# Optimization experiments

Hardware: AMD Instinct MI355X
Metric: run time of the kernel (lower is better)

## Reference

```python
import jax, jax.numpy as jnp
import numpy as np

B, T, D, K = 8, 4096, 1024, 3


def setup_inputs() -> dict:
    key = jax.random.key(0)
    k0, k1, k2 = jax.random.split(key, 3)
    x = jax.random.normal(k0, (B, T, D), dtype=jnp.float32)
    lim = 1.0 / np.sqrt(D)
    Wv = jax.random.uniform(k1, (D, D), dtype=jnp.float32, minval=-lim, maxval=lim)
    bv = jnp.zeros((D,), dtype=jnp.float32)
    Wo = jax.random.uniform(k2, (D, D), dtype=jnp.float32, minval=-lim, maxval=lim)
    bo = jnp.zeros((D,), dtype=jnp.float32)
    neighbor_weights = jnp.ones((K,), dtype=jnp.float32) / K
    return {"x": x, "Wv": Wv, "bv": bv, "Wo": Wo, "bo": bo,
            "neighbor_weights": neighbor_weights}


def reference(x, Wv, bv, Wo, bo, neighbor_weights):
    # x: [B, T, D]; faithful translation of the unfold -> Linear -> weighted-sum chain
    k = neighbor_weights.shape[0]
    pad = k // 2
    t = x.shape[1]
    # replicate padding along T (torch F.pad mode='replicate')
    xp = jnp.pad(x, ((0, 0), (pad, pad), (0, 0)), mode='edge')  # [B, T+2*pad, D]
    # sliding windows: [B, T, K, D] (small fixed K loop, not a data-dim loop)
    windows = jnp.stack([xp[:, i:i + t, :] for i in range(k)], axis=2)
    # value projection applied per window element (nn.Linear: x @ W.T + b)
    v = jnp.einsum('btkd,ed->btke', windows, Wv) + bv  # [B, T, K, D]
    # fixed-weight neighbor average
    attended = jnp.einsum('btkd,k->btd', v, neighbor_weights)  # [B, T, D]
    # output projection
    return jnp.einsum('btd,ed->bte', attended, Wo) + bo
```

## Files before the change

### kernel.cpp

```cpp
#include <hip/hip_runtime.h>
#include <stdint.h>
#include <stddef.h>

typedef _Float16 f16_t;
typedef _Float16 f16x4 __attribute__((ext_vector_type(4)));
typedef _Float16 f16x8 __attribute__((ext_vector_type(8)));
typedef float f32x4 __attribute__((ext_vector_type(4)));

#define AS_G __attribute__((address_space(1)))
#define AS_L __attribute__((address_space(3)))

__device__ __forceinline__ void gload_lds16(const void* g, void* l) {
  __builtin_amdgcn_global_load_lds((AS_G void*)g, (AS_L void*)l, 16, 0, 0);
}

#define FENCE() asm volatile("" ::: "memory")
#define BARX()                            \
  do {                                    \
    FENCE();                              \
    __builtin_amdgcn_s_barrier();         \
    FENCE();                              \
  } while (0)
#define VMCNT(n) asm volatile("s_waitcnt vmcnt(" #n ")" ::: "memory")


__global__ __launch_bounds__(256) void prep_w_kernel(
    const float* __restrict__ Wo, const float* __restrict__ Wv,
    const float* __restrict__ bv, const float* __restrict__ bo,
    const float* __restrict__ nw, int Kw,
    f16_t* __restrict__ Wo_h, f16_t* __restrict__ WvT, float* __restrict__ bc) {
  __shared__ float smem[32 * 33];
  const int b = blockIdx.x;
  const int t = threadIdx.x;
  if (b < 1024) {
    const int i = b * 256 + t;
    f32x4 v = ((const f32x4*)Wo)[i];
    f16x4 o;
    o.x = (f16_t)v.x; o.y = (f16_t)v.y; o.z = (f16_t)v.z; o.w = (f16_t)v.w;
    ((f16x4*)Wo_h)[i] = o;
  } else if (b < 2048) {
    const int i = b - 1024;
    const int bx = i & 31, by = i >> 5;
    const int tx = t & 31, ty = t >> 5;
#pragma unroll
    for (int k = 0; k < 32; k += 8)
      smem[(ty + k) * 33 + tx] = Wv[(size_t)(by * 32 + ty + k) * 1024 + bx * 32 + tx];
    __syncthreads();
#pragma unroll
    for (int k = 0; k < 32; k += 8)
      WvT[(size_t)(bx * 32 + ty + k) * 1024 + by * 32 + tx] = (f16_t)smem[tx * 33 + ty + k];
  } else {
    const int e = b - 2048;
    float sw = 0.f;
    for (int k = 0; k < Kw; ++k) sw += nw[k];
    float p = 0.f;
    for (int d = t; d < 1024; d += 256) p += Wo[(size_t)e * 1024 + d] * bv[d];
    smem[t] = p;
    __syncthreads();
    for (int s = 128; s > 0; s >>= 1) {
      if (t < s) smem[t] += smem[t + s];
      __syncthreads();
    }
    if (t == 0) bc[e] = sw * smem[0] + bo[e];
  }
}


__global__ __launch_bounds__(256) void xavg_wct_kernel(
    const float* __restrict__ X, const float* __restrict__ nw,
    const f16_t* __restrict__ Wo_h, const f16_t* __restrict__ WvT,
    f16_t* __restrict__ Xavg, f16_t* __restrict__ WcT) {
  __shared__ __align__(16) f16_t smem[2 * 128 * 32];
  const int b = blockIdx.x;
  const int tid = threadIdx.x;

  if (b < 4096) {
    const int T = 4096, D = 1024;
    const int base = b * 8;
    const int t0 = base & (T - 1);
    const int col = tid * 4;
    const float w0 = nw[0], w1 = nw[1], w2 = nw[2];
    const float* xb = X + (size_t)base * D + col;
    f32x4 va = *(const f32x4*)(xb + (t0 == 0 ? 0 : -D));
    f32x4 vb = *(const f32x4*)(xb);
    f16_t* ob = Xavg + (size_t)base * D + col;
#pragma unroll
    for (int g = 0; g < 8; ++g) {
      f32x4 vc;
      if (t0 + g == T - 1) vc = vb;
      else vc = *(const f32x4*)(xb + (size_t)(g + 1) * D);
      f32x4 y = w0 * va + w1 * vb + w2 * vc;
      f16x4 o;
      o.x = (f16_t)y.x; o.y = (f16_t)y.y; o.z = (f16_t)y.z; o.w = (f16_t)y.w;
      *(f16x4*)(ob + (size_t)g * D) = o;
      va = vb;
      vb = vc;
    }
    return;
  }

  constexpr int K = 1024, N = 1024;
  f16_t* sA = smem;
  f16_t* sB = smem + 128 * 32;
  const int l = tid & 63;
  const int w = tid >> 6;
  const int wr = w >> 1;
  const int wc = w & 1;
  const int bid = b - 4096;
  const int mt = bid & 7;
  const int nt = bid >> 3;
  const int m0 = mt << 7;
  const int n0 = nt << 7;

  const int srow = (w << 4) + (l >> 2);
  const int scol = (l & 3) << 3;
  const size_t aoff0 = (size_t)(m0 + srow) * K + scol;
  const size_t boff0 = (size_t)(n0 + srow) * K + scol;
  f16_t* ldsA = sA + (w << 9);
  f16_t* ldsB = sB + (w << 9);

  f32x4 acc[4][4];
#pragma unroll
  for (int i = 0; i < 4; ++i)
#pragma unroll
    for (int j = 0; j < 4; ++j) acc[i][j] = f32x4{0.f, 0.f, 0.f, 0.f};

  const int ka = (l >> 4) << 3;
  const int ar = (wr << 6) + (l & 15);
  const int br = (wc << 6) + (l & 15);

  for (int kt = 0; kt < (K >> 5); ++kt) {
    const int kb = kt << 5;
    gload_lds16(Wo_h + aoff0 + kb, ldsA);
    gload_lds16(Wo_h + aoff0 + ((size_t)K << 6) + kb, ldsA + 2048);
    gload_lds16(WvT + boff0 + kb, ldsB);
    gload_lds16(WvT + boff0 + ((size_t)K << 6) + kb, ldsB + 2048);
    __syncthreads();
    f16x8 af[4], bfr[4];
#pragma unroll
    for (int m = 0; m < 4; ++m) af[m] = *(const f16x8*)(sA + ((ar + (m << 4)) << 5) + ka);
#pragma unroll
    for (int n = 0; n < 4; ++n) bfr[n] = *(const f16x8*)(sB + ((br + (n << 4)) << 5) + ka);
#pragma unroll
    for (int m = 0; m < 4; ++m)
#pragma unroll
      for (int n = 0; n < 4; ++n)
        acc[m][n] = __builtin_amdgcn_mfma_f32_16x16x32_f16(af[m], bfr[n], acc[m][n], 0, 0, 0);
    __syncthreads();
  }

  const int orow = (l >> 4) << 2;
  const int ocol = l & 15;
#pragma unroll
  for (int n = 0; n < 4; ++n) {
    const int gn = n0 + (wc << 6) + (n << 4) + ocol;
#pragma unroll
    for (int m = 0; m < 4; ++m) {
      const int gm = m0 + (wr << 6) + (m << 4) + orow;
#pragma unroll
      for (int j = 0; j < 4; ++j) {
        WcT[(size_t)(gm + j) * N + gn] = (f16_t)acc[m][n][j];
      }
    }
  }
}


__device__ __forceinline__ void stage256(const f16_t* __restrict__ g, int K,
                                         f16_t* ldsOp, int w, int l) {
#pragma unroll
  for (int i = 0; i < 2; ++i) {
    const int f = i * 512 + w * 64 + l;
    const int row = f >> 2;
    const int ch = f & 3;
    const int col = (((ch ^ ((row >> 1) & 3))) << 3);
    gload_lds16(g + (size_t)row * K + col, ldsOp + i * 4096 + w * 512);
  }
}

__global__ __launch_bounds__(512, 2) void gemm256_kernel(const f16_t* __restrict__ A,
                                                         const f16_t* __restrict__ Bt,
                                                         float* __restrict__ C,
                                                         const float* __restrict__ bias,
                                                         int M, int N, int K) {
  __shared__ __align__(16) f16_t lds[4 * 16384];
  const int tid = threadIdx.x;
  const int l = tid & 63;
  const int w = tid >> 6;
  const int wr = w >> 2;
  const int wc = w & 3;
  const int lr = l & 15;
  const int q = l >> 4;

  const int cpx = (int)gridDim.x >> 3;
  const int swzb = ((int)blockIdx.x & 7) * cpx + ((int)blockIdx.x >> 3);
  const int nNT = N >> 8;
  const int mt = swzb / nNT;
  const int nt = swzb % nNT;
  const int m0 = mt << 8;
  const int n0 = nt << 8;

  const f16_t* Apanel = A + (size_t)m0 * K;
  const f16_t* Bpanel = Bt + (size_t)n0 * K;
  const int sw = (q ^ ((lr >> 1) & 3)) << 3;

  f32x4 acc[8][4];
#pragma unroll
  for (int m = 0; m < 8; ++m)
#pragma unroll
    for (int n = 0; n < 4; ++n) acc[m][n] = f32x4{0.f, 0.f, 0.f, 0.f};

  const int nK = K >> 5;

  for (int t = 0; t < 3; ++t) {
    f16_t* buf = lds + (t & 3) * 16384;
    stage256(Apanel + (t << 5), K, buf, w, l);
    stage256(Bpanel + (t << 5), K, buf + 8192, w, l);
  }
  VMCNT(8);
  BARX();

  for (int t = 0; t < nK; ++t) {
    f16_t* sA = lds + (t & 3) * 16384;
    f16_t* sB = sA + 8192;

    {
      const int tn = (t + 3) < nK ? (t + 3) : (nK - 1);
      f16_t* nbuf = lds + ((t + 3) & 3) * 16384;
      stage256(Apanel + ((size_t)tn << 5), K, nbuf, w, l);
      stage256(Bpanel + ((size_t)tn << 5), K, nbuf + 8192, w, l);
    }

    f16x8 bf[4], af[4], ag[4];
#pragma unroll
    for (int n = 0; n < 4; ++n)
      bf[n] = *(const f16x8*)(sB + (((wc << 6) + (n << 4) + lr) << 5) + sw);
#pragma unroll
    for (int m = 0; m < 4; ++m)
      af[m] = *(const f16x8*)(sA + (((wr << 7) + (m << 4) + lr) << 5) + sw);
#pragma unroll
    for (int m = 0; m < 4; ++m)
      ag[m] = *(const f16x8*)(sA + (((wr << 7) + 64 + (m << 4) + lr) << 5) + sw);

    __builtin_amdgcn_s_setprio(1);
#pragma unroll
    for (int m = 0; m < 4; ++m)
#pragma unroll
      for (int n = 0; n < 4; ++n)
        acc[m][n] = __builtin_amdgcn_mfma_f32_16x16x32_f16(af[m], bf[n], acc[m][n], 0, 0, 0);
#pragma unroll
    for (int m = 0; m < 4; ++m)
#pragma unroll
      for (int n = 0; n < 4; ++n)
        acc[m + 4][n] = __builtin_amdgcn_mfma_f32_16x16x32_f16(ag[m], bf[n], acc[m + 4][n], 0, 0, 0);
    __builtin_amdgcn_s_setprio(0);

    VMCNT(8);
    BARX();
  }

  float bs[4];
#pragma unroll
  for (int n = 0; n < 4; ++n) bs[n] = bias[n0 + (wc << 6) + (n << 4) + lr];
#pragma unroll
  for (int m = 0; m < 8; ++m) {
    const int gm = m0 + (wr << 7) + (m << 4) + (q << 2);
#pragma unroll
    for (int j = 0; j < 4; ++j) {
      float* Crow = C + (size_t)(gm + j) * N + n0 + (wc << 6) + lr;
#pragma unroll
      for (int n = 0; n < 4; ++n) Crow[n << 4] = acc[m][n][j] + bs[n];
    }
  }
}


extern "C" void kernel_launch(void* const* d_in, const int* in_sizes, int n_in,
                              void* d_out, int out_size, void* d_ws, size_t ws_size,
                              hipStream_t stream) {
  const float* x = (const float*)d_in[0];
  const float* Wv = (const float*)d_in[1];
  const float* bv = (const float*)d_in[2];
  const float* Wo = (const float*)d_in[3];
  const float* bo = (const float*)d_in[4];
  const float* nw = (const float*)d_in[5];
  float* out = (float*)d_out;

  char* ws = (char*)d_ws;
  f16_t* Wo_h = (f16_t*)(ws);
  f16_t* WvT  = (f16_t*)(ws + (2u << 20));
  f16_t* WcT  = (f16_t*)(ws + (4u << 20));
  float* bc   = (float*)(ws + (6u << 20));
  f16_t* Xavg = (f16_t*)(ws + (8u << 20));

  prep_w_kernel<<<dim3(3072), dim3(256), 0, stream>>>(
      Wo, Wv, bv, bo, nw, in_sizes[5], Wo_h, WvT, bc);
  xavg_wct_kernel<<<dim3(4160), dim3(256), 0, stream>>>(
      x, nw, Wo_h, WvT, Xavg, WcT);
  gemm256_kernel<<<dim3(512), dim3(512), 0, stream>>>(
      Xavg, WcT, out, bc, 32768, 1024, 1024);
}
```

Measured before the change: 145.1 us.

## Fuse weight prep into Xavg/WcT kernel, converting fp32 weights in-tile

New measurement: 161.4 us. +11.3%, slower.

```diff
diff --git a/kernel.cpp b/kernel.cpp
--- a/kernel.cpp
+++ b/kernel.cpp
@@ -6,6 +6,7 @@
 typedef _Float16 f16x4 __attribute__((ext_vector_type(4)));
 typedef _Float16 f16x8 __attribute__((ext_vector_type(8)));
 typedef float f32x4 __attribute__((ext_vector_type(4)));
+typedef float f32x8 __attribute__((ext_vector_type(8)));
 
 #define AS_G __attribute__((address_space(1)))
 #define AS_L __attribute__((address_space(3)))
@@ -24,144 +25,119 @@
 #define VMCNT(n) asm volatile("s_waitcnt vmcnt(" #n ")" ::: "memory")
 
 
-__global__ __launch_bounds__(256) void prep_w_kernel(
-    const float* __restrict__ Wo, const float* __restrict__ Wv,
-    const float* __restrict__ bv, const float* __restrict__ bo,
-    const float* __restrict__ nw, int Kw,
-    f16_t* __restrict__ Wo_h, f16_t* __restrict__ WvT, float* __restrict__ bc) {
-  __shared__ float smem[32 * 33];
+__global__ __launch_bounds__(256) void prep_fused_kernel(
+    const float* __restrict__ X, const float* __restrict__ Wo,
+    const float* __restrict__ Wv, const float* __restrict__ bv,
+    const float* __restrict__ bo, const float* __restrict__ nw, int Kw,
+    f16_t* __restrict__ Xavg, f16_t* __restrict__ WcT, float* __restrict__ bc) {
+  __shared__ __align__(16) f16_t sA[128 * 32];
+  __shared__ __align__(16) float sWv[32 * 132];
+  __shared__ float smem[256];
   const int b = blockIdx.x;
-  const int t = threadIdx.x;
-  if (b < 1024) {
-    const int i = b * 256 + t;
-    f32x4 v = ((const f32x4*)Wo)[i];
-    f16x4 o;
-    o.x = (f16_t)v.x; o.y = (f16_t)v.y; o.z = (f16_t)v.z; o.w = (f16_t)v.w;
-    ((f16x4*)Wo_h)[i] = o;
-  } else if (b < 2048) {
-    const int i = b - 1024;
-    const int bx = i & 31, by = i >> 5;
-    const int tx = t & 31, ty = t >> 5;
-#pragma unroll
-    for (int k = 0; k < 32; k += 8)
-      smem[(ty + k) * 33 + tx] = Wv[(size_t)(by * 32 + ty + k) * 1024 + bx * 32 + tx];
-    __syncthreads();
-#pragma unroll
-    for (int k = 0; k < 32; k += 8)
-      WvT[(size_t)(bx * 32 + ty + k) * 1024 + by * 32 + tx] = (f16_t)smem[tx * 33 + ty + k];
+  const int tid = threadIdx.x;
+
+  if (b < 4096) {
+    const int T = 4096, D = 1024;
+    const int base = b * 8;
+    const int bb = (base >> 12) << 12;
+    const int be = bb + T - 1;
+    const int half = tid >> 7;
+    const int c8 = (tid & 127) * 8;
+    const float w0 = nw[0], w1 = nw[1], w2 = nw[2];
+#pragma unroll
+    for (int g = 0; g < 4; ++g) {
+      const int r = base + 2 * g + half;
+      const int rm = (r > bb) ? r - 1 : bb;
+      const int rp = (r < be) ? r + 1 : be;
+      f32x8 a = *(const f32x8*)(X + (size_t)rm * D + c8);
+      f32x8 v = *(const f32x8*)(X + (size_t)r * D + c8);
+      f32x8 c = *(const f32x8*)(X + (size_t)rp * D + c8);
+      f32x8 y = w0 * a + w1 * v + w2 * c;
+      f16x8 o;
+#pragma unroll
+      for (int e = 0; e < 8; ++e) o[e] = (f16_t)y[e];
+      *(f16x8*)(Xavg + (size_t)r * D + c8) = o;
+    }
+  } else if (b < 4160) {
+    constexpr int K = 1024, NN = 1024;
+    const int bid = b - 4096;
+    const int mt = bid & 7, nt = bid >> 3;
+    const int m0 = mt << 7, n0 = nt << 7;
+    const int l = tid & 63, w = tid >> 6;
+    const int wr = w >> 1, wc = w & 1;
+    const int ka = (l >> 4) << 3;
+    const int ar = (wr << 6) + (l & 15);
+    const int br = (wc << 6) + (l & 15);
+
+    f32x4 acc[4][4];
+#pragma unroll
+    for (int i = 0; i < 4; ++i)
+#pragma unroll
+      for (int j = 0; j < 4; ++j) acc[i][j] = f32x4{0.f, 0.f, 0.f, 0.f};
+
+    for (int kt = 0; kt < (K >> 5); ++kt) {
+      const int kb = kt << 5;
+#pragma unroll
+      for (int i = 0; i < 2; ++i) {
+        const int u = tid + i * 256;
+        const int row = u >> 2, ch = u & 3;
+        f32x8 v = *(const f32x8*)(Wo + (size_t)(m0 + row) * K + kb + ch * 8);
+        f16x8 h;
+#pragma unroll
+        for (int e = 0; e < 8; ++e) h[e] = (f16_t)v[e];
+        *(f16x8*)(sA + row * 32 + ch * 8) = h;
+      }
+#pragma unroll
+      for (int i = 0; i < 4; ++i) {
+        const int u = tid + i * 256;
+        const int k = u >> 5, c4 = u & 31;
+        f32x4 v = *(const f32x4*)(Wv + (size_t)(kb + k) * NN + n0 + c4 * 4);
+        *(f32x4*)(sWv + k * 132 + c4 * 4) = v;
+      }
+      __syncthreads();
+      f16x8 af[4], bfr[4];
+#pragma unroll
+      for (int m = 0; m < 4; ++m) af[m] = *(const f16x8*)(sA + (ar + (m << 4)) * 32 + ka);
+#pragma unroll
+      for (int n = 0; n < 4; ++n) {
+#pragma unroll
+        for (int e = 0; e < 8; ++e)
+          bfr[n][e] = (f16_t)sWv[(ka + e) * 132 + br + (n << 4)];
+      }
+#pragma unroll
+      for (int m = 0; m < 4; ++m)
+#pragma unroll
+        for (int n = 0; n < 4; ++n)
+          acc[m][n] = __builtin_amdgcn_mfma_f32_16x16x32_f16(af[m], bfr[n], acc[m][n], 0, 0, 0);
+      __syncthreads();
+    }
+
+    const int orow = (l >> 4) << 2;
+    const int ocol = l & 15;
+#pragma unroll
+    for (int n = 0; n < 4; ++n) {
+      const int gn = n0 + (wc << 6) + (n << 4) + ocol;
+#pragma unroll
+      for (int m = 0; m < 4; ++m) {
+        const int gm = m0 + (wr << 6) + (m << 4) + orow;
+#pragma unroll
+        for (int j = 0; j < 4; ++j)
+          WcT[(size_t)(gm + j) * NN + gn] = (f16_t)acc[m][n][j];
+      }
+    }
   } else {
-    const int e = b - 2048;
+    const int e = b - 4160;
     float sw = 0.f;
     for (int k = 0; k < Kw; ++k) sw += nw[k];
     float p = 0.f;
-    for (int d = t; d < 1024; d += 256) p += Wo[(size_t)e * 1024 + d] * bv[d];
-    smem[t] = p;
+    for (int d = tid; d < 1024; d += 256) p += Wo[(size_t)e * 1024 + d] * bv[d];
+    smem[tid] = p;
     __syncthreads();
     for (int s = 128; s > 0; s >>= 1) {
-      if (t < s) smem[t] += smem[t + s];
+      if (tid < s) smem[tid] += smem[tid + s];
       __syncthreads();
     }
-    if (t == 0) bc[e] = sw * smem[0] + bo[e];
-  }
-}
-
-
-__global__ __launch_bounds__(256) void xavg_wct_kernel(
-    const float* __restrict__ X, const float* __restrict__ nw,
-    const f16_t* __restrict__ Wo_h, const f16_t* __restrict__ WvT,
-    f16_t* __restrict__ Xavg, f16_t* __restrict__ WcT) {
-  __shared__ __align__(16) f16_t smem[2 * 128 * 32];
-  const int b = blockIdx.x;
-  const int tid = threadIdx.x;
-
-  if (b < 4096) {
-    const int T = 4096, D = 1024;
-    const int base = b * 8;
-    const int t0 = base & (T - 1);
-    const int col = tid * 4;
-    const float w0 = nw[0], w1 = nw[1], w2 = nw[2];
-    const float* xb = X + (size_t)base * D + col;
-    f32x4 va = *(const f32x4*)(xb + (t0 == 0 ? 0 : -D));
-    f32x4 vb = *(const f32x4*)(xb);
-    f16_t* ob = Xavg + (size_t)base * D + col;
-#pragma unroll
-    for (int g = 0; g < 8; ++g) {
-      f32x4 vc;
-      if (t0 + g == T - 1) vc = vb;
-      else vc = *(const f32x4*)(xb + (size_t)(g + 1) * D);
-      f32x4 y = w0 * va + w1 * vb + w2 * vc;
-      f16x4 o;
-      o.x = (f16_t)y.x; o.y = (f16_t)y.y; o.z = (f16_t)y.z; o.w = (f16_t)y.w;
-      *(f16x4*)(ob + (size_t)g * D) = o;
-      va = vb;
-      vb = vc;
-    }
-    return;
-  }
-
-  constexpr int K = 1024, N = 1024;
-  f16_t* sA = smem;
-  f16_t* sB = smem + 128 * 32;
-  const int l = tid & 63;
-  const int w = tid >> 6;
-  const int wr = w >> 1;
-  const int wc = w & 1;
-  const int bid = b - 4096;
-  const int mt = bid & 7;
-  const int nt = bid >> 3;
-  const int m0 = mt << 7;
-  const int n0 = nt << 7;
-
-  const int srow = (w << 4) + (l >> 2);
-  const int scol = (l & 3) << 3;
-  const size_t aoff0 = (size_t)(m0 + srow) * K + scol;
-  const size_t boff0 = (size_t)(n0 + srow) * K + scol;
-  f16_t* ldsA = sA + (w << 9);
-  f16_t* ldsB = sB + (w << 9);
-
-  f32x4 acc[4][4];
-#pragma unroll
-  for (int i = 0; i < 4; ++i)
-#pragma unroll
-    for (int j = 0; j < 4; ++j) acc[i][j] = f32x4{0.f, 0.f, 0.f, 0.f};
-
-  const int ka = (l >> 4) << 3;
-  const int ar = (wr << 6) + (l & 15);
-  const int br = (wc << 6) + (l & 15);
-
-  for (int kt = 0; kt < (K >> 5); ++kt) {
-    const int kb = kt << 5;
-    gload_lds16(Wo_h + aoff0 + kb, ldsA);
-    gload_lds16(Wo_h + aoff0 + ((size_t)K << 6) + kb, ldsA + 2048);
-    gload_lds16(WvT + boff0 + kb, ldsB);
-    gload_lds16(WvT + boff0 + ((size_t)K << 6) + kb, ldsB + 2048);
-    __syncthreads();
-    f16x8 af[4], bfr[4];
-#pragma unroll
-    for (int m = 0; m < 4; ++m) af[m] = *(const f16x8*)(sA + ((ar + (m << 4)) << 5) + ka);
-#pragma unroll
-    for (int n = 0; n < 4; ++n) bfr[n] = *(const f16x8*)(sB + ((br + (n << 4)) << 5) + ka);
-#pragma unroll
-    for (int m = 0; m < 4; ++m)
-#pragma unroll
-      for (int n = 0; n < 4; ++n)
-        acc[m][n] = __builtin_amdgcn_mfma_f32_16x16x32_f16(af[m], bfr[n], acc[m][n], 0, 0, 0);
-    __syncthreads();
-  }
-
-  const int orow = (l >> 4) << 2;
-  const int ocol = l & 15;
-#pragma unroll
-  for (int n = 0; n < 4; ++n) {
-    const int gn = n0 + (wc << 6) + (n << 4) + ocol;
-#pragma unroll
-    for (int m = 0; m < 4; ++m) {
-      const int gm = m0 + (wr << 6) + (m << 4) + orow;
-#pragma unroll
-      for (int j = 0; j < 4; ++j) {
-        WcT[(size_t)(gm + j) * N + gn] = (f16_t)acc[m][n][j];
-      }
-    }
+    if (tid == 0) bc[e] = sw * smem[0] + bo[e];
   }
 }
 
@@ -287,16 +263,12 @@
   float* out = (float*)d_out;
 
   char* ws = (char*)d_ws;
-  f16_t* Wo_h = (f16_t*)(ws);
-  f16_t* WvT  = (f16_t*)(ws + (2u << 20));
   f16_t* WcT  = (f16_t*)(ws + (4u << 20));
   float* bc   = (float*)(ws + (6u << 20));
   f16_t* Xavg = (f16_t*)(ws + (8u << 20));
 
-  prep_w_kernel<<<dim3(3072), dim3(256), 0, stream>>>(
-      Wo, Wv, bv, bo, nw, in_sizes[5], Wo_h, WvT, bc);
-  xavg_wct_kernel<<<dim3(4160), dim3(256), 0, stream>>>(
-      x, nw, Wo_h, WvT, Xavg, WcT);
+  prep_fused_kernel<<<dim3(5184), dim3(256), 0, stream>>>(
+      x, Wo, Wv, bv, bo, nw, in_sizes[5], Xavg, WcT, bc);
   gemm256_kernel<<<dim3(512), dim3(512), 0, stream>>>(
       Xavg, WcT, out, bc, 32768, 1024, 1024);
 }
```
